# Kernel optimization log

Measured on AMD Instinct MI355X. Metric: run time of the kernel, lower is better.

The kernel has to match this reference:

```python
import jax, jax.numpy as jnp
from jax import lax
import numpy as np

MASK_PROBABILITY = 0.65
MASK_SPAN = 10
# per-position Bernoulli prob after dividing by span (as in __init__)
P_SPARSE = MASK_PROBABILITY / MASK_SPAN
# span split, exactly as in calculate_mask
STEPS_AFTER = (MASK_SPAN - 1) // 2 if (MASK_SPAN - 1) % 2 == 0 else MASK_SPAN // 2
STEPS_BEFORE = MASK_SPAN - STEPS_AFTER - 1


def setup_inputs() -> dict:
    key = jax.random.key(0)
    k1, k2 = jax.random.split(key)
    seq = jax.random.normal(k1, (16, 4096, 512), dtype=jnp.float32)
    mask_item = jax.random.normal(k2, (1, 512), dtype=jnp.float32)
    return {"seq": seq, "mask_item": mask_item}


def _calculate_mask(B, S):
    # Bernoulli sparse midpoints [B, S]
    key = jax.random.key(42)
    sparse = jax.random.bernoulli(key, P_SPARSE, (B, S)).astype(jnp.int32)
    # Dilate: position j becomes 1 if any midpoint m in [j-STEPS_AFTER, j+STEPS_BEFORE]
    # (a midpoint m covers [m-STEPS_BEFORE, m+STEPS_AFTER]). Fused 1D max-pool via reduce_window.
    dilated = lax.reduce_window(
        sparse, 0, lax.max,
        window_dimensions=(1, MASK_SPAN), window_strides=(1, 1),
        padding=[(0, 0), (STEPS_AFTER, STEPS_BEFORE)],
    )
    # Torch quirk: slice end is min(m + STEPS_AFTER + 1, S - 1), so the last position
    # is never set by dilation -- only by the sparse sample itself.
    is_last = (jnp.arange(S) == S - 1)[None, :]
    mask = jnp.where(is_last, sparse, dilated)
    return mask.astype(bool)


def reference(seq, mask_item):
    B, S, C = seq.shape
    mask = _calculate_mask(B, S)  # [B, S] bool
    # masked scatter of the learned mask embedding (single fused where)
    out = jnp.where(mask[:, :, None], mask_item[0].astype(seq.dtype), seq)
    # Original returns mask_ids = nonzero(mask) (dynamic shape); we return the dense
    # boolean mask (as int32) instead for jit-compatibility -- same information.
    return out, mask.astype(jnp.int32)
```

## Files before the change

kernel.cpp:

```cpp
#include <hip/hip_runtime.h>

#define BB 16
#define SS 4096
#define CC 512
#define NPOS (BB * SS)
#define OUT_ELEMS (BB * SS * CC)
#define N4 (OUT_ELEMS / 4)

__device__ __forceinline__ unsigned rotl32(unsigned x, unsigned d) {
    return (x << d) | (x >> (32u - d));
}

__device__ __forceinline__ unsigned threefry_bits(unsigned i) {
    const unsigned k0 = 0u;
    const unsigned k1 = 42u;
    const unsigned k2 = 0u ^ 42u ^ 0x1BD11BDAu;
    unsigned v0 = 0u + k0;
    unsigned v1 = i + k1;

#define TF_RND(r) { v0 += v1; v1 = rotl32(v1, (r)); v1 ^= v0; }
    TF_RND(13) TF_RND(15) TF_RND(26) TF_RND(6)
    v0 += k1; v1 += k2 + 1u;
    TF_RND(17) TF_RND(29) TF_RND(16) TF_RND(24)
    v0 += k2; v1 += k0 + 2u;
    TF_RND(13) TF_RND(15) TF_RND(26) TF_RND(6)
    v0 += k0; v1 += k1 + 3u;
    TF_RND(17) TF_RND(29) TF_RND(16) TF_RND(24)
    v0 += k1; v1 += k2 + 4u;
    TF_RND(13) TF_RND(15) TF_RND(26) TF_RND(6)
    v0 += k2; v1 += k0 + 5u;
#undef TF_RND

    return v0 ^ v1;
}

__device__ __forceinline__ int sparse_at(int i) {
    unsigned bits = threefry_bits((unsigned)i);
    unsigned fb = (bits >> 9) | 0x3f800000u;
    float u = __uint_as_float(fb) - 1.0f;
    return (u < 0.065f) ? 1 : 0;
}

__global__ __launch_bounds__(256) void mask_kernel(float* __restrict__ maskf) {
    __shared__ int sp[256 + 10];
    const int base = blockIdx.x * 256;
    const int rowstart = base & ~(SS - 1);

    for (int k = threadIdx.x; k < 266; k += 256) {
        int p = base - 5 + k;
        int v = 0;
        if (p >= rowstart && p < rowstart + SS) v = sparse_at(p);
        sp[k] = v;
    }
    __syncthreads();

    const int i = base + threadIdx.x;
    const int j = i & (SS - 1);
    int m;
    if (j == SS - 1) {
        m = sp[threadIdx.x + 5];
    } else {
        m = 0;
#pragma unroll
        for (int w = 0; w < 10; ++w) m |= sp[threadIdx.x + w];
    }
    maskf[i] = (float)m;
}

__global__ __launch_bounds__(256) void apply_kernel(const float4* __restrict__ seq,
                                                    const float4* __restrict__ mi,
                                                    const float* __restrict__ maskf,
                                                    float4* __restrict__ out) {
    const int stride = gridDim.x * blockDim.x;
    for (int i = blockIdx.x * blockDim.x + threadIdx.x; i < N4; i += stride) {
        const int pos = i >> 7;
        float4 v;
        if (maskf[pos] != 0.0f) {
            v = mi[i & 127];
        } else {
            v = seq[i];
        }
        out[i] = v;
    }
}

extern "C" void kernel_launch(void* const* d_in, const int* in_sizes, int n_in,
                              void* d_out, int out_size, void* d_ws, size_t ws_size,
                              hipStream_t stream) {
    const float* seq = (const float*)d_in[0];
    const float* mask_item = (const float*)d_in[1];
    float* out = (float*)d_out;
    float* maskf = out + OUT_ELEMS;

    mask_kernel<<<NPOS / 256, 256, 0, stream>>>(maskf);
    apply_kernel<<<2048, 256, 0, stream>>>((const float4*)seq,
                                           (const float4*)mask_item,
                                           maskf,
                                           (float4*)out);
}
```

Before: 40.24 us.

## Fuse mask generation into apply kernel with nontemporal loads and stores

Merges the separate mask-generation and apply kernels into a single kernel where each block computes the dilated mask for its 32 positions in shared memory and then writes the corresponding output rows. This removes one kernel launch and the global round trip of the mask between kernels. Loads from seq and stores to out use nontemporal builtins to avoid cache pollution for streaming data. The tradeoff is a per-block serial prologue (threefry plus two barriers) with few active threads before the streaming copy begins.

```diff
diff --git a/kernel.cpp b/kernel.cpp
--- a/kernel.cpp
+++ b/kernel.cpp
@@ -5,7 +5,12 @@
 #define CC 512
 #define NPOS (BB * SS)
 #define OUT_ELEMS (BB * SS * CC)
-#define N4 (OUT_ELEMS / 4)
+
+#define POS_PER_BLK 32
+#define F4_PER_POS (CC / 4)
+#define F4_PER_BLK (POS_PER_BLK * F4_PER_POS)
+
+typedef float vfloat4 __attribute__((ext_vector_type(4)));
 
 __device__ __forceinline__ unsigned rotl32(unsigned x, unsigned d) {
     return (x << d) | (x >> (32u - d));
@@ -41,46 +46,48 @@
     return (u < 0.065f) ? 1 : 0;
 }
 
-__global__ __launch_bounds__(256) void mask_kernel(float* __restrict__ maskf) {
-    __shared__ int sp[256 + 10];
-    const int base = blockIdx.x * 256;
+__global__ __launch_bounds__(256) void fused_kernel(const vfloat4* __restrict__ seq,
+                                                    const vfloat4* __restrict__ mi,
+                                                    float* __restrict__ maskf,
+                                                    vfloat4* __restrict__ out) {
+    __shared__ int sp[POS_PER_BLK + 9];
+    __shared__ int msk[POS_PER_BLK];
+
+    const int base = blockIdx.x * POS_PER_BLK;
     const int rowstart = base & ~(SS - 1);
+    const int t = threadIdx.x;
 
-    for (int k = threadIdx.x; k < 266; k += 256) {
-        int p = base - 5 + k;
-        int v = 0;
-        if (p >= rowstart && p < rowstart + SS) v = sparse_at(p);
-        sp[k] = v;
+    if (t < POS_PER_BLK + 9) {
+        int p = base - 5 + t;
+        sp[t] = (p >= rowstart && p < rowstart + SS) ? sparse_at(p) : 0;
     }
     __syncthreads();
 
-    const int i = base + threadIdx.x;
-    const int j = i & (SS - 1);
-    int m;
-    if (j == SS - 1) {
-        m = sp[threadIdx.x + 5];
-    } else {
-        m = 0;
+    if (t < POS_PER_BLK) {
+        const int j = (base + t) & (SS - 1);
+        int m;
+        if (j == SS - 1) {
+            m = sp[t + 5];
+        } else {
+            m = 0;
 #pragma unroll
-        for (int w = 0; w < 10; ++w) m |= sp[threadIdx.x + w];
+            for (int w = 0; w < 10; ++w) m |= sp[t + w];
+        }
+        msk[t] = m;
+        maskf[base + t] = (float)m;
     }
-    maskf[i] = (float)m;
-}
+    __syncthreads();
 
-__global__ __launch_bounds__(256) void apply_kernel(const float4* __restrict__ seq,
-                                                    const float4* __restrict__ mi,
-                                                    const float* __restrict__ maskf,
-                                                    float4* __restrict__ out) {
-    const int stride = gridDim.x * blockDim.x;
-    for (int i = blockIdx.x * blockDim.x + threadIdx.x; i < N4; i += stride) {
-        const int pos = i >> 7;
-        float4 v;
-        if (maskf[pos] != 0.0f) {
-            v = mi[i & 127];
+    const long long blk_f4 = (long long)blockIdx.x * F4_PER_BLK;
+#pragma unroll
+    for (int k = t; k < F4_PER_BLK; k += 256) {
+        vfloat4 v;
+        if (msk[k >> 7]) {
+            v = mi[k & (F4_PER_POS - 1)];
         } else {
-            v = seq[i];
+            v = __builtin_nontemporal_load(&seq[blk_f4 + k]);
         }
-        out[i] = v;
+        __builtin_nontemporal_store(v, &out[blk_f4 + k]);
     }
 }
 
@@ -92,9 +99,8 @@
     float* out = (float*)d_out;
     float* maskf = out + OUT_ELEMS;
 
-    mask_kernel<<<NPOS / 256, 256, 0, stream>>>(maskf);
-    apply_kernel<<<2048, 256, 0, stream>>>((const float4*)seq,
-                                           (const float4*)mask_item,
-                                           maskf,
-                                           (float4*)out);
+    fused_kernel<<<NPOS / POS_PER_BLK, 256, 0, stream>>>((const vfloat4*)seq,
+                                                         (const vfloat4*)mask_item,
+                                                         maskf,
+                                                         (vfloat4*)out);
 }
```

Measured after the change: 36.94 us. 1.09x faster.
